# Kernel optimization log

Hardware: AMD Instinct MI355X
Metric: run time of the kernel (lower is better)

Reference implementation:

```python
import jax, jax.numpy as jnp
import numpy as np

B, CIN, COUT, WID, M1, M2, H, W = 8, 3, 3, 16, 8, 8, 256, 256


def _fftfreq(n, d):
    # torch.fft.fftfreq(n, d); d may be a traced scalar
    k = np.concatenate([np.arange(0, (n - 1) // 2 + 1), np.arange(-(n // 2), 0)]).astype(np.float32)
    return jnp.asarray(k) / (n * d)


def _cplx(ri):
    return jax.lax.complex(ri[..., 0], ri[..., 1])


def _inorm(v, eps=1e-5):
    # InstanceNorm2d, affine=False: normalize over spatial dims per (b, c)
    mu = jnp.mean(v, axis=(-2, -1), keepdims=True)
    var = jnp.var(v, axis=(-2, -1), keepdims=True)
    return (v - mu) * jax.lax.rsqrt(var + eps)


def setup_inputs() -> dict:
    key = jax.random.key(0)
    ks = jax.random.split(key, 13)
    scale = 1.0 / (WID * WID)
    u = lambda k, s: scale * (0.5 + 0.5 * jax.random.uniform(k, s, jnp.float32))
    return {
        "x": jax.random.normal(ks[0], (B, CIN, H, W), jnp.float32),
        "fc0_w": jax.random.normal(ks[1], (CIN + 2, WID), jnp.float32) * 0.1,
        "fc0_b": jax.random.normal(ks[2], (WID,), jnp.float32) * 0.01,
        "pole1_ri": u(ks[3], (WID, WID, M1, 2)),
        "pole2_ri": u(ks[4], (WID, WID, M2, 2)),
        "residue_ri": u(ks[5], (WID, WID, M1, M2, 2)),
        "w0_w": jax.random.normal(ks[6], (WID, WID), jnp.float32) * 0.1,
        "w0_b": jax.random.normal(ks[7], (WID,), jnp.float32) * 0.01,
        "fc1_w": jax.random.normal(ks[8], (WID, 128), jnp.float32) * 0.1,
        "fc1_b": jax.random.normal(ks[9], (128,), jnp.float32) * 0.01,
        "fc2_w": jax.random.normal(ks[10], (128, COUT), jnp.float32) * 0.1,
        "fc2_b": jax.random.normal(ks[11], (COUT,), jnp.float32) * 0.01,
        "tx": jnp.linspace(0.0, 1.0, W, dtype=jnp.float32).reshape(1, W),
        "ty": jnp.linspace(0.0, 1.0, H, dtype=jnp.float32).reshape(1, H),
    }


def _pr2d(v, p1, p2, res, tx, ty):
    # v: [b, i, h, w] real; p1:[i,k,m1], p2:[i,k,m2], res:[i,k,m1,m2] complex
    b, i, h, w = v.shape
    dty = ty[0, 1] - ty[0, 0]
    dtx = tx[0, 1] - tx[0, 0]
    alpha = jnp.fft.fft2(v)  # [b,i,h,w] complex64
    lam1 = (2j * jnp.pi) * _fftfreq(h, dty)  # [h]
    lam2 = (2j * jnp.pi) * _fftfreq(w, dtx)  # [w]
    A1 = 1.0 / (lam1[None, None, None, :] - p1[..., None])  # [i,k,p,h]
    A2 = 1.0 / (lam2[None, None, None, :] - p2[..., None])  # [i,k,q,w]
    # output_residue1[b,k,o,x] = sum_{i,p,q} alpha[b,i,o,x] res[i,k,p,q] A1[i,k,p,o] A2[i,k,q,x]
    T = jnp.einsum('ikpq,ikpo->ikqo', res, A1)
    G = jnp.einsum('ikqo,ikqx->ikox', T, A2)        # [i,k,h,w] pole-residue transfer kernel
    out1 = jnp.einsum('biox,ikox->bkox', alpha, G)
    x1 = jnp.fft.ifft2(out1).real
    # output_residue2[b,k,p,q] = sum_{i,o,x} alpha[b,i,o,x] res[i,k,p,q] A1[i,k,p,o] A2[i,k,q,x]
    S = jnp.einsum('biox,ikqx->bikoq', alpha, A2)
    Mt = jnp.einsum('bikoq,ikpo->bikpq', S, A1)
    out2 = jnp.einsum('bikpq,ikpq->bkpq', Mt, res)  # [b,k,m1,m2]
    # transient part: x2[n,i,z,x] = sum_{b,p,q} out2[n,b,p,q] exp(p1[b,i,p] ty[z]) exp(p2[b,i,q] tx[x])
    tyc = ty.reshape(-1).astype(p1.dtype)
    txc = tx.reshape(-1).astype(p2.dtype)
    E1 = jnp.exp(p1[..., None] * tyc)  # [i,k,p,h]
    E2 = jnp.exp(p2[..., None] * txc)  # [i,k,q,w]
    U = jnp.einsum('nbpq,bipz->nbiqz', out2, E1)
    x2 = jnp.einsum('nbiqz,biqx->nizx', U, E2).real / (w * h)
    return x1 + x2


def reference(x, fc0_w, fc0_b, pole1_ri, pole2_ri, residue_ri, w0_w, w0_b,
              fc1_w, fc1_b, fc2_w, fc2_b, tx, ty):
    b, c, h, w = x.shape
    v = jnp.transpose(x, (0, 2, 3, 1))  # [b,h,w,c]
    gx = jnp.broadcast_to(jnp.linspace(0.0, 1.0, h, dtype=x.dtype)[None, :, None, None], (b, h, w, 1))
    gy = jnp.broadcast_to(jnp.linspace(0.0, 1.0, w, dtype=x.dtype)[None, None, :, None], (b, h, w, 1))
    v = jnp.concatenate([v, gx, gy], axis=-1)
    v = v @ fc0_w + fc0_b                 # [b,h,w,width]
    v = jnp.transpose(v, (0, 3, 1, 2))    # [b,width,h,w]
    p1, p2, res = _cplx(pole1_ri), _cplx(pole2_ri), _cplx(residue_ri)
    x1 = _inorm(_pr2d(_inorm(v), p1, p2, res, tx, ty))
    x2 = jnp.einsum('bihw,oi->bohw', v, w0_w) + w0_b[None, :, None, None]  # 1x1 conv
    u = x1 + x2
    u = jnp.transpose(u, (0, 2, 3, 1))
    u = jnp.sin(u @ fc1_w + fc1_b)
    u = u @ fc2_w + fc2_b
    return jnp.transpose(u, (0, 3, 1, 2))
```

## Files before the change

### kernel.cpp

```cpp
#include <hip/hip_runtime.h>
#include <cstddef>

#define NPIX 65536
#define PI_F 3.14159265358979323846f

typedef float v4f __attribute__((ext_vector_type(4)));
typedef short v8s __attribute__((ext_vector_type(8)));
typedef unsigned short u16;

__device__ __forceinline__ void cacc(float2& acc, float2 a, float2 b) {
  acc.x = fmaf(a.x, b.x, fmaf(-a.y, b.y, acc.x));
  acc.y = fmaf(a.x, b.y, fmaf(a.y, b.x, acc.y));
}
__device__ __forceinline__ float2 cmulf(float2 a, float2 b) {
  return make_float2(a.x*b.x - a.y*b.y, a.x*b.y + a.y*b.x);
}
__device__ __forceinline__ float2 add2(float2 a, float2 b) { return make_float2(a.x+b.x, a.y+b.y); }
__device__ __forceinline__ float2 sub2(float2 a, float2 b) { return make_float2(a.x-b.x, a.y-b.y); }
__device__ __forceinline__ float2 shflc(float2 v, int mask) {
  return make_float2(__shfl_xor(v.x, mask), __shfl_xor(v.y, mask));
}
__device__ __forceinline__ void nts2(float2* p, float2 v) {
  __builtin_nontemporal_store(*reinterpret_cast<const double*>(&v),
                              reinterpret_cast<double*>(p));
}
__device__ __forceinline__ void nts1(float* p, float v) {
  __builtin_nontemporal_store(v, p);
}
__device__ __forceinline__ void bf16split(float v, u16& h, u16& l) {
  unsigned bits = __float_as_uint(v);
  h = (u16)(bits >> 16);
  float r = v - __uint_as_float((unsigned)h << 16);
  l = (u16)(__float_as_uint(r) >> 16);
}
__device__ __forceinline__ void make_tw(float sgn, int l, float2* tw) {
  const float c = sgn * (2.0f*PI_F/256.0f);
  int idxs[8] = { l, 64+l, 2*l, (l&31)<<2, (l&15)<<3, (l&7)<<4, (l&3)<<5, (l&1)<<6 };
  #pragma unroll
  for (int r = 0; r < 8; ++r) { float sn, cs; __sincosf(c*idxs[r], &sn, &cs); tw[r] = make_float2(cs, sn); }
}
__device__ __forceinline__ void fwd_stage(float2& vv, int lane, int H, float2 tws, bool unit) {
  float2 p = shflc(vv, H);
  bool up = (lane & H) != 0;
  float2 lo = add2(vv, p);
  float2 df = sub2(p, vv);
  float2 hi = unit ? df : cmulf(df, tws);
  vv = up ? hi : lo;
}
__device__ __forceinline__ void inv_stage(float2& vv, int lane, int H, float2 tws, bool unit) {
  float2 p = shflc(vv, H);
  bool up = (lane & H) != 0;
  float2 bv = up ? vv : p;
  float2 av = up ? p : vv;
  float2 t = unit ? bv : cmulf(bv, tws);
  vv = up ? sub2(av, t) : add2(av, t);
}
__device__ __forceinline__ void ifft256_reg(float2& v0, float2& v1, float2& v2,
    float2& v3, int lane, const float2* tw) {
  inv_stage(v0, lane, 1, tw[0], true ); inv_stage(v1, lane, 1, tw[0], true );
  inv_stage(v2, lane, 1, tw[0], true ); inv_stage(v3, lane, 1, tw[0], true );
  inv_stage(v0, lane, 2, tw[7], false); inv_stage(v1, lane, 2, tw[7], false);
  inv_stage(v2, lane, 2, tw[7], false); inv_stage(v3, lane, 2, tw[7], false);
  inv_stage(v0, lane, 4, tw[6], false); inv_stage(v1, lane, 4, tw[6], false);
  inv_stage(v2, lane, 4, tw[6], false); inv_stage(v3, lane, 4, tw[6], false);
  inv_stage(v0, lane, 8, tw[5], false); inv_stage(v1, lane, 8, tw[5], false);
  inv_stage(v2, lane, 8, tw[5], false); inv_stage(v3, lane, 8, tw[5], false);
  inv_stage(v0, lane, 16, tw[4], false); inv_stage(v1, lane, 16, tw[4], false);
  inv_stage(v2, lane, 16, tw[4], false); inv_stage(v3, lane, 16, tw[4], false);
  inv_stage(v0, lane, 32, tw[3], false); inv_stage(v1, lane, 32, tw[3], false);
  inv_stage(v2, lane, 32, tw[3], false); inv_stage(v3, lane, 32, tw[3], false);
  { float2 t01 = cmulf(v1, tw[2]); float2 n0 = add2(v0, t01), n1 = sub2(v0, t01);
    float2 t23 = cmulf(v3, tw[2]); float2 n2 = add2(v2, t23), n3 = sub2(v2, t23);
    v0 = n0; v1 = n1; v2 = n2; v3 = n3; }
  { float2 t02 = cmulf(v2, tw[0]); float2 n0 = add2(v0, t02), n2 = sub2(v0, t02);
    float2 t13 = cmulf(v3, tw[1]); float2 n1 = add2(v1, t13), n3 = sub2(v1, t13);
    v0 = n0; v2 = n2; v1 = n1; v3 = n3; }
}

__global__ __launch_bounds__(256) void k_setup(const float2* __restrict__ p1,
    const float2* __restrict__ p2, const float* __restrict__ txv,
    const float* __restrict__ tyv, float2* __restrict__ A1,
    float2* __restrict__ A2T, float2* __restrict__ A2L,
    float2* __restrict__ E1, float2* __restrict__ E2) {
  int gid = blockIdx.x*256 + threadIdx.x;
  int o = gid & 255, p = (gid>>8)&7, k = (gid>>11)&15, i = gid>>15;
  float ko = (o < 128) ? (float)o : (float)(o - 256);
  float dty = tyv[1] - tyv[0];
  float dtx = txv[1] - txv[0];
  const float TWO_PI = 6.283185307179586f;
  {
    float lam = TWO_PI * ko / (256.0f * dty);
    float2 pv = p1[(i*16+k)*8 + p];
    float xr = -pv.x, yi = lam - pv.y;
    float D = xr*xr + yi*yi;
    A1[((size_t)((i*16+k)*8 + p))*256 + o] = make_float2(xr/D, -yi/D);
    float tv = tyv[o];
    float m = expf(pv.x*tv);
    E1[((size_t)((i*16+k)*8 + p))*256 + o] = make_float2(m*cosf(pv.y*tv), m*sinf(pv.y*tv));
  }
  {
    int fo = __brev((unsigned)o) >> 24;
    float ko2 = (fo < 128) ? (float)fo : (float)(fo - 256);
    float lam = TWO_PI * ko2 / (256.0f * dtx);
    float2 pv = p2[(i*16+k)*8 + p];
    float xr = -pv.x, yi = lam - pv.y;
    float D = xr*xr + yi*yi;
    float2 val = make_float2(xr/D, -yi/D);
    A2T[((size_t)i*256 + o)*128 + k*8 + p] = val;
    A2L[((size_t)((i*16+k)*8 + p))*256 + o] = val;
    float tv = txv[o];
    float m = expf(pv.x*tv);
    E2[((size_t)((i*16+k)*8 + p))*256 + o] = make_float2(m*cosf(pv.y*tv), m*sinf(pv.y*tv));
  }
}

__global__ __launch_bounds__(256) void k_B(const float2* __restrict__ A2T,
    u16* __restrict__ BH, u16* __restrict__ BL) {
  int bid = blockIdx.x;
  int i = bid >> 3, g = bid & 7;
  int tid = threadIdx.x;
  int n2 = g*32 + (tid >> 3);
  int kq = n2 >> 1, par = n2 & 1;
  int x0 = (tid & 7) * 32;
  size_t outb = ((size_t)i*256 + n2)*512;
  for (int xx = 0; xx < 32; ++xx) {
    int x = x0 + xx;
    float2 a2 = A2T[((size_t)i*256 + x)*128 + kq];
    float v0 = par ? a2.y : a2.x;
    float v1 = par ? a2.x : -a2.y;
    u16 h0, l0, h1, l1;
    bf16split(v0, h0, l0);
    bf16split(v1, h1, l1);
    BH[outb + 2*x]     = h0;  BL[outb + 2*x]     = l0;
    BH[outb + 2*x + 1] = h1;  BL[outb + 2*x + 1] = l1;
  }
}

__global__ __launch_bounds__(256) void k_T(const float2* __restrict__ res,
    const float2* __restrict__ A1, float2* __restrict__ Tt) {
  int ik = blockIdx.x, tid = threadIdx.x;
  __shared__ float2 rbuf[64];
  __shared__ float2 a1[8][256];
  if (tid < 64) rbuf[tid] = res[(size_t)ik*64 + tid];
  for (int e = 0; e < 8; ++e) {
    int lin = tid + 256*e;
    int p = lin >> 8, o = lin & 255;
    a1[p][o] = A1[((size_t)ik*8 + p)*256 + o];
  }
  __syncthreads();
  int o = tid;
  #pragma unroll
  for (int q = 0; q < 8; ++q) {
    float2 acc = make_float2(0.f, 0.f);
    #pragma unroll
    for (int p = 0; p < 8; ++p) cacc(acc, rbuf[p*8+q], a1[p][o]);
    Tt[((size_t)ik*8 + q)*256 + o] = acc;
  }
}

__global__ __launch_bounds__(256) void k_stats_v_part(const float* __restrict__ x,
    const float* __restrict__ fc0w, const float* __restrict__ fc0b,
    float2* __restrict__ part) {
  int bid = blockIdx.x;
  int seg = bid & 7, img = bid >> 3;
  int k = img & 15, b = img >> 4;
  int tid = threadIdx.x;
  float w0 = fc0w[k], w1 = fc0w[16+k], w2 = fc0w[32+k], w3 = fc0w[48+k], w4 = fc0w[64+k];
  float base = fc0b[k] + (tid*(1.0f/255.0f))*w4;
  const float* xb = x + (size_t)b*3*NPIX + (size_t)seg*8192;
  float s = 0.f, s2 = 0.f;
  for (int it = 0; it < 32; ++it) {
    int row = seg*32 + it;
    int p = it*256 + tid;
    float val = base + (row*(1.0f/255.0f))*w3 + xb[p]*w0 + xb[NPIX+p]*w1 + xb[2*NPIX+p]*w2;
    s += val; s2 += val*val;
  }
  __shared__ float rs[256], rq[256];
  rs[tid] = s; rq[tid] = s2;
  __syncthreads();
  for (int off = 128; off > 0; off >>= 1) {
    if (tid < off) { rs[tid] += rs[tid+off]; rq[tid] += rq[tid+off]; }
    __syncthreads();
  }
  if (tid == 0) part[bid] = make_float2(rs[0], rq[0]);
}

__global__ __launch_bounds__(256) void k_stats_p_part(const float* __restrict__ v,
    float2* __restrict__ part) {
  int bid = blockIdx.x;
  int seg = bid & 7, img = bid >> 3;
  int tid = threadIdx.x;
  const float* p = v + (size_t)img*NPIX + (size_t)seg*8192;
  float s = 0.f, s2 = 0.f;
  for (int it = 0; it < 32; ++it) { float a = p[it*256 + tid]; s += a; s2 += a*a; }
  __shared__ float rs[256], rq[256];
  rs[tid] = s; rq[tid] = s2;
  __syncthreads();
  for (int off = 128; off > 0; off >>= 1) {
    if (tid < off) { rs[tid] += rs[tid+off]; rq[tid] += rq[tid+off]; }
    __syncthreads();
  }
  if (tid == 0) part[bid] = make_float2(rs[0], rq[0]);
}

__global__ __launch_bounds__(256) void k_stats_fin(const float2* __restrict__ part,
    float2* __restrict__ stats, int nimg) {
  int img = blockIdx.x*256 + threadIdx.x;
  if (img >= nimg) return;
  float s = 0.f, s2 = 0.f;
  #pragma unroll
  for (int e = 0; e < 8; ++e) { float2 v = part[img*8 + e]; s += v.x; s2 += v.y; }
  float mean = s * (1.0f/65536.0f);
  float var  = s2 * (1.0f/65536.0f) - mean*mean;
  stats[img] = make_float2(mean, rsqrtf(var + 1e-5f));
}

__global__ __launch_bounds__(256) void k_fft_v(const float* __restrict__ x,
    const float* __restrict__ fc0w, const float* __restrict__ fc0b,
    const float2* __restrict__ stats, float2* __restrict__ out) {
  int tid = threadIdx.x, lane = tid & 63, rowi = tid >> 6;
  int bid = blockIdx.x;
  int img = bid >> 6;
  int h   = (bid & 63)*4 + rowi;
  int k = img & 15, b = img >> 4;
  float2 st = stats[img];
  float w0 = fc0w[k], w1 = fc0w[16+k], w2 = fc0w[32+k], w3 = fc0w[48+k], w4 = fc0w[64+k];
  float bb = fc0b[k] + (h*(1.0f/255.0f))*w3;
  const float* xb = x + (size_t)b*3*NPIX + (size_t)h*256;
  float2 tw[8];
  make_tw(-1.0f, lane, tw);
  float2 v0, v1, v2, v3;
  {
    #pragma unroll
    for (int e = 0; e < 4; ++e) {
      int j = e*64 + lane;
      float val = bb + (j*(1.0f/255.0f))*w4 + xb[j]*w0 + xb[NPIX+j]*w1 + xb[2*NPIX+j]*w2;
      val = (val - st.x)*st.y;
      float2 c = make_float2(val, 0.f);
      if (e == 0) v0 = c; else if (e == 1) v1 = c; else if (e == 2) v2 = c; else v3 = c;
    }
  }
  { float2 n0 = add2(v0, v2), n2 = cmulf(sub2(v0, v2), tw[0]);
    float2 n1 = add2(v1, v3), n3 = cmulf(sub2(v1, v3), tw[1]);
    v0 = n0; v1 = n1; v2 = n2; v3 = n3; }
  { float2 n0 = add2(v0, v1), n1 = cmulf(sub2(v0, v1), tw[2]);
    float2 n2 = add2(v2, v3), n3 = cmulf(sub2(v2, v3), tw[2]);
    v0 = n0; v1 = n1; v2 = n2; v3 = n3; }
  fwd_stage(v0, lane, 32, tw[3], false); fwd_stage(v1, lane, 32, tw[3], false);
  fwd_stage(v2, lane, 32, tw[3], false); fwd_stage(v3, lane, 32, tw[3], false);
  fwd_stage(v0, lane, 16, tw[4], false); fwd_stage(v1, lane, 16, tw[4], false);
  fwd_stage(v2, lane, 16, tw[4], false); fwd_stage(v3, lane, 16, tw[4], false);
  fwd_stage(v0, lane,  8, tw[5], false); fwd_stage(v1, lane,  8, tw[5], false);
  fwd_stage(v2, lane,  8, tw[5], false); fwd_stage(v3, lane,  8, tw[5], false);
  fwd_stage(v0, lane,  4, tw[6], false); fwd_stage(v1, lane,  4, tw[6], false);
  fwd_stage(v2, lane,  4, tw[6], false); fwd_stage(v3, lane,  4, tw[6], false);
  fwd_stage(v0, lane,  2, tw[7], false); fwd_stage(v1, lane,  2, tw[7], false);
  fwd_stage(v2, lane,  2, tw[7], false); fwd_stage(v3, lane,  2, tw[7], false);
  fwd_stage(v0, lane,  1, tw[0], true ); fwd_stage(v1, lane,  1, tw[0], true );
  fwd_stage(v2, lane,  1, tw[0], true ); fwd_stage(v3, lane,  1, tw[0], true );
  float2* op = out + ((size_t)img*256 + h)*256;
  nts2(&op[lane], v0); nts2(&op[64+lane], v1);
  nts2(&op[128+lane], v2); nts2(&op[192+lane], v3);
}

__global__ __launch_bounds__(256) void k_fft_colR(const float2* __restrict__ in,
    float2* __restrict__ outp) {
  __shared__ float tr[256][17], tim[256][17];
  __shared__ float twr[128], twi[128];
  int tid = threadIdx.x;
  int c = tid & 15, g = tid >> 4;
  int img = blockIdx.x >> 4;
  int c0  = (blockIdx.x & 15) * 16;
  if (tid < 128) {
    float ang = (PI_F/128.0f)*tid;
    twr[tid] = cosf(ang); twi[tid] = -sinf(ang);
  }
  const float2* base = in + (size_t)img*NPIX + c0;
  #pragma unroll
  for (int it = 0; it < 16; ++it) {
    int row = it*16 + g;
    float2 v = base[(size_t)row*256 + c];
    int br = __brev((unsigned)row) >> 24;
    tr[br][c] = v.x; tim[br][c] = v.y;
  }
  __syncthreads();
  int lane = tid & 63, w = tid >> 6;
  int cw = w*4 + (lane >> 4);
  int gw = lane & 15;
  for (int s = 0; s < 8; ++s) {
    __builtin_amdgcn_wave_barrier();
    int half = 1 << s;
    #pragma unroll
    for (int r = 0; r < 8; ++r) {
      int m  = gw + 16*r;
      int t  = m & (half - 1);
      int grp = m >> s;
      int i0 = (grp << (s+1)) + t;
      int i1 = i0 + half;
      int twx = t << (7 - s);
      float wr = twr[twx], wi = twi[twx];
      float br = tr[i1][cw], bi = tim[i1][cw];
      float vr = br*wr - bi*wi, vi = br*wi + bi*wr;
      float ar = tr[i0][cw], ai = tim[i0][cw];
      tr[i0][cw] = ar + vr; tim[i0][cw] = ai + vi;
      tr[i1][cw] = ar - vr; tim[i1][cw] = ai - vi;
    }
  }
  __syncthreads();
  #pragma unroll
  for (int it = 0; it < 16; ++it) {
    int row = it*16 + g;
    float2 vv = make_float2(tr[row][c], tim[row][c]);
    nts2(&outp[((size_t)row*128 + img)*256 + c0 + c], vv);
  }
}

__global__ __launch_bounds__(256) void k_ifft_col_real(const float2* __restrict__ in,
    float* __restrict__ outp, float scale) {
  __shared__ float tr[256][17], tim[256][17];
  __shared__ float twr[128], twi[128];
  int tid = threadIdx.x;
  int c = tid & 15, g = tid >> 4;
  int img = blockIdx.x >> 4;
  int c0  = (blockIdx.x & 15) * 16;
  if (tid < 128) {
    float ang = (PI_F/128.0f)*tid;
    twr[tid] = cosf(ang); twi[tid] = sinf(ang);
  }
  const float2* base = in + (size_t)img*NPIX + c0;
  #pragma unroll
  for (int it = 0; it < 16; ++it) {
    int row = it*16 + g;
    float2 v = base[(size_t)row*256 + c];
    int br = __brev((unsigned)row) >> 24;
    tr[br][c] = v.x; tim[br][c] = v.y;
  }
  __syncthreads();
  int lane = tid & 63, w = tid >> 6;
  int cw = w*4 + (lane >> 4);
  int gw = lane & 15;
  for (int s = 0; s < 8; ++s) {
    __builtin_amdgcn_wave_barrier();
    int half = 1 << s;
    #pragma unroll
    for (int r = 0; r < 8; ++r) {
      int m  = gw + 16*r;
      int t  = m & (half - 1);
      int grp = m >> s;
      int i0 = (grp << (s+1)) + t;
      int i1 = i0 + half;
      int twx = t << (7 - s);
      float wr = twr[twx], wi = twi[twx];
      float br = tr[i1][cw], bi = tim[i1][cw];
      float vr = br*wr - bi*wi, vi = br*wi + bi*wr;
      float ar = tr[i0][cw], ai = tim[i0][cw];
      tr[i0][cw] = ar + vr; tim[i0][cw] = ai + vi;
      tr[i1][cw] = ar - vr; tim[i1][cw] = ai - vi;
    }
  }
  __syncthreads();
  float* ob = outp + (size_t)img*NPIX + c0;
  #pragma unroll
  for (int it = 0; it < 16; ++it) {
    int row = it*16 + g;
    nts1(&ob[(size_t)row*256 + c], tr[row][c]*scale);
  }
}

__global__ __launch_bounds__(256) void k_Smm(const float2* __restrict__ alphaR,
    const u16* __restrict__ BH, const u16* __restrict__ BL,
    float* __restrict__ Sf) {
  __shared__ u16 Ah[128][40], Al[128][40], Bhs[128][40], Bls[128][40];
  int bid = blockIdx.x;
  int i = bid >> 5, rem = bid & 31, mt = rem >> 1, nt = rem & 1;
  int tid = threadIdx.x;
  int lane = tid & 63, wid = tid >> 6, wr = wid >> 1, wc = wid & 1;
  int r2 = tid >> 1, h2 = tid & 1;
  int m_s = mt*128 + r2;
  const float2* arow = alphaR + ((size_t)((m_s & 255)*128) + (size_t)((m_s >> 8)*16 + i))*256 + h2*8;
  const u16* bhrow = BH + ((size_t)i*256 + nt*128 + r2)*512 + h2*16;
  const u16* blrow = BL + ((size_t)i*256 + nt*128 + r2)*512 + h2*16;
  v4f acc[4][4];
  #pragma unroll
  for (int a = 0; a < 4; ++a)
    #pragma unroll
    for (int b = 0; b < 4; ++b) acc[a][b] = (v4f){0.f, 0.f, 0.f, 0.f};
  for (int kc = 0; kc < 16; ++kc) {
    const float2* ap = arow + kc*16;
    #pragma unroll
    for (int e = 0; e < 8; ++e) {
      float2 v = ap[e];
      u16 hr, lr, hi_, li_;
      bf16split(v.x, hr, lr);
      bf16split(v.y, hi_, li_);
      int c = h2*16 + 2*e;
      Ah[r2][c] = hr; Ah[r2][c+1] = hi_;
      Al[r2][c] = lr; Al[r2][c+1] = li_;
    }
    {
      const uint4* ph = (const uint4*)(bhrow + (size_t)kc*32);
      uint4 q0 = ph[0], q1 = ph[1];
      *((uint4*)&Bhs[r2][h2*16])     = q0;
      *((uint4*)&Bhs[r2][h2*16 + 8]) = q1;
      const uint4* pl = (const uint4*)(blrow + (size_t)kc*32);
      uint4 s0 = pl[0], s1 = pl[1];
      *((uint4*)&Bls[r2][h2*16])     = s0;
      *((uint4*)&Bls[r2][h2*16 + 8]) = s1;
    }
    __syncthreads();
    v8s af_h[4], af_l[4];
    int c8 = (lane >> 4) * 8;
    #pragma unroll
    for (int fi = 0; fi < 4; ++fi) {
      int row = wr*64 + fi*16 + (lane & 15);
      af_h[fi] = *(const v8s*)&Ah[row][c8];
      af_l[fi] = *(const v8s*)&Al[row][c8];
    }
    #pragma unroll
    for (int fj = 0; fj < 4; ++fj) {
      int row = wc*64 + fj*16 + (lane & 15);
      v8s bh_f = *(const v8s*)&Bhs[row][c8];
      v8s bl_f = *(const v8s*)&Bls[row][c8];
      #pragma unroll
      for (int fi = 0; fi < 4; ++fi) {
        acc[fi][fj] = __builtin_amdgcn_mfma_f32_16x16x32_bf16(af_h[fi], bh_f, acc[fi][fj], 0, 0, 0);
        acc[fi][fj] = __builtin_amdgcn_mfma_f32_16x16x32_bf16(af_l[fi], bh_f, acc[fi][fj], 0, 0, 0);
        acc[fi][fj] = __builtin_amdgcn_mfma_f32_16x16x32_bf16(af_h[fi], bl_f, acc[fi][fj], 0, 0, 0);
      }
    }
    __syncthreads();
  }
  #pragma unroll
  for (int fi = 0; fi < 4; ++fi) {
    #pragma unroll
    for (int rr = 0; rr < 4; ++rr) {
      int m = mt*128 + wr*64 + fi*16 + (lane >> 4)*4 + rr;
      int n = m >> 8, o = m & 255;
      float* srow = Sf + ((size_t)(n*16 + i)*256 + o)*256 + nt*128 + wc*64 + (lane & 15);
      #pragma unroll
      for (int fj = 0; fj < 4; ++fj)
        nts1(&srow[fj*16], acc[fi][fj][rr]);
    }
  }
}

__global__ __launch_bounds__(256) void k_Mt(const float2* __restrict__ S,
    const float2* __restrict__ A1, float2* __restrict__ Mt) {
  __shared__ float2 sl[8][258];
  __shared__ float2 a1l[8][258];
  __shared__ float2 part[4][64];
  int bid = blockIdx.x;
  int k = bid & 15, ni = bid >> 4;
  int i = ni & 15;
  int ik = i*16 + k;
  int tid = threadIdx.x;
  for (int e = 0; e < 8; ++e) {
    int lin = tid + 256*e;
    int o = lin >> 3, q = lin & 7;
    sl[q][o] = S[((size_t)ni*256 + o)*128 + k*8 + q];
  }
  for (int e = 0; e < 8; ++e) {
    int lin = tid + 256*e;
    int p = lin >> 8, o = lin & 255;
    a1l[p][o] = A1[((size_t)ik*8 + p)*256 + o];
  }
  __syncthreads();
  int oq = tid >> 6, pq = tid & 63, p = pq >> 3, q = pq & 7;
  float2 acc = make_float2(0.f, 0.f);
  int o0 = oq*64;
  for (int o = o0; o < o0 + 64; ++o) cacc(acc, sl[q][o], a1l[p][o]);
  part[oq][pq] = acc;
  __syncthreads();
  if (oq == 0) {
    float2 a = part[0][pq], b = part[1][pq], c = part[2][pq], d = part[3][pq];
    acc.x = a.x + b.x + c.x + d.x;
    acc.y = a.y + b.y + c.y + d.y;
    Mt[(size_t)bid*64 + pq] = acc;
  }
}

__global__ __launch_bounds__(256) void k_out2(const float2* __restrict__ Mt,
    const float2* __restrict__ res, float2* __restrict__ out2) {
  int gid = blockIdx.x*256 + threadIdx.x;
  int pq = gid & 63, k = (gid >> 6) & 15, n = gid >> 10;
  float2 acc = make_float2(0.f, 0.f);
  for (int i = 0; i < 16; ++i)
    cacc(acc, Mt[((size_t)((n*16+i)*16 + k))*64 + pq], res[((size_t)(i*16+k))*64 + pq]);
  out2[((size_t)(n*16+k))*64 + pq] = acc;
}

__global__ __launch_bounds__(256) void k_out1g(const float2* __restrict__ alphaR,
    const float2* __restrict__ Tt, const float2* __restrict__ A2L,
    float2* __restrict__ out1) {
  __shared__ float2 tl[2][128];
  __shared__ float sre[4][256], sim[4][256];
  int d = blockIdx.x;
  int xcd = d & 7, idx = d >> 3;
  int o  = xcd*32 + (idx >> 3);
  int kh = idx & 7;
  int tid = threadIdx.x, x = tid;
  int lane = tid & 63, rowi = tid >> 6;
  {
    int kk = tid >> 7, rem = tid & 127;
    int i = rem >> 3, q = rem & 7;
    tl[kk][rem] = Tt[((size_t)((i*16 + 2*kh + kk)*8 + q))*256 + o];
  }
  float2 tw[8];
  make_tw(+1.0f, lane, tw);
  __syncthreads();
  float2 g0[16], g1[16];
  #pragma unroll
  for (int i = 0; i < 16; ++i) {
    const float2* a2k0 = &A2L[((size_t)((i*16 + 2*kh + 0)*8))*256 + x];
    const float2* a2k1 = &A2L[((size_t)((i*16 + 2*kh + 1)*8))*256 + x];
    float2 acc0 = make_float2(0.f, 0.f), acc1 = make_float2(0.f, 0.f);
    #pragma unroll
    for (int q = 0; q < 8; ++q) {
      cacc(acc0, tl[0][i*8+q], a2k0[(size_t)q*256]);
      cacc(acc1, tl[1][i*8+q], a2k1[(size_t)q*256]);
    }
    g0[i] = acc0; g1[i] = acc1;
  }
  const float2* arow = alphaR + (size_t)o*128*256 + x;
  float2 arA[16], arB[16];
  #pragma unroll
  for (int i = 0; i < 16; ++i) arA[i] = arow[(size_t)(0*16 + i)*256];
  #pragma unroll
  for (int i = 0; i < 16; ++i) arB[i] = arow[(size_t)(1*16 + i)*256];
  for (int bp = 0; bp < 4; ++bp) {
    float2 acc0 = make_float2(0.f,0.f), acc1 = acc0, acc2 = acc0, acc3 = acc0;
    #pragma unroll
    for (int i = 0; i < 16; ++i) {
      cacc(acc0, arA[i], g0[i]);
      cacc(acc1, arA[i], g1[i]);
      cacc(acc2, arB[i], g0[i]);
      cacc(acc3, arB[i], g1[i]);
    }
    sre[0][x] = acc0.x; sim[0][x] = acc0.y;
    sre[1][x] = acc1.x; sim[1][x] = acc1.y;
    sre[2][x] = acc2.x; sim[2][x] = acc2.y;
    sre[3][x] = acc3.x; sim[3][x] = acc3.y;
    __syncthreads();
    if (bp < 3) {
      int b0 = (bp+1)*2, b1 = b0 + 1;
      #pragma unroll
      for (int i = 0; i < 16; ++i) arA[i] = arow[(size_t)(b0*16 + i)*256];
      #pragma unroll
      for (int i = 0; i < 16; ++i) arB[i] = arow[(size_t)(b1*16 + i)*256];
    }
    float2 v0 = make_float2(sre[rowi][lane],     sim[rowi][lane]);
    float2 v1 = make_float2(sre[rowi][64+lane],  sim[rowi][64+lane]);
    float2 v2 = make_float2(sre[rowi][128+lane], sim[rowi][128+lane]);
    float2 v3 = make_float2(sre[rowi][192+lane], sim[rowi][192+lane]);
    ifft256_reg(v0, v1, v2, v3, lane, tw);
    int img = (bp*2 + (rowi >> 1))*16 + 2*kh + (rowi & 1);
    float2* op = out1 + ((size_t)img*256 + o)*256;
    nts2(&op[lane], v0); nts2(&op[64+lane], v1);
    nts2(&op[128+lane], v2); nts2(&op[192+lane], v3);
    __syncthreads();
  }
}

__global__ __launch_bounds__(256) void k_x2t(const float2* __restrict__ out2,
    const float2* __restrict__ E1, const float2* __restrict__ E2,
    float* __restrict__ x1pre) {
  int bid = blockIdx.x;
  int zb = bid & 31, nk = bid >> 5;
  int kk = nk & 15, n = nk >> 4;
  int x = threadIdx.x;
  __shared__ float2 o2[1024];
  __shared__ float2 e1l[1024];
  __shared__ float2 ul[1024];
  for (int e = 0; e < 4; ++e) {
    int lin = threadIdx.x + 256*e;
    int j = lin >> 6, pq = lin & 63;
    o2[lin] = out2[((size_t)(n*16 + j))*64 + pq];
  }
  for (int e = 0; e < 4; ++e) {
    int lin = threadIdx.x + 256*e;
    int j = lin >> 6, p = (lin >> 3) & 7, zz = lin & 7;
    e1l[lin] = E1[(((size_t)(j*16 + kk))*8 + p)*256 + zb*8 + zz];
  }
  __syncthreads();
  for (int e = 0; e < 4; ++e) {
    int lin = threadIdx.x + 256*e;
    int j = lin >> 6, q = (lin >> 3) & 7, zz = lin & 7;
    float2 acc = make_float2(0.f, 0.f);
    #pragma unroll
    for (int p = 0; p < 8; ++p) cacc(acc, o2[j*64 + p*8 + q], e1l[j*64 + p*8 + zz]);
    ul[lin] = acc;
  }
  __syncthreads();
  float acc[8] = {0.f,0.f,0.f,0.f,0.f,0.f,0.f,0.f};
  const float2* e2b = E2 + (size_t)kk*2048 + x;
  float2 nxt = e2b[0];
  for (int jq = 0; jq < 128; ++jq) {
    float2 e2 = nxt;
    int njq = jq + 1;
    if (njq < 128) {
      int nj = njq >> 3, nq = njq & 7;
      nxt = e2b[(size_t)nj*32768 + (size_t)nq*256];
    }
    const float4* up4 = reinterpret_cast<const float4*>(&ul[jq*8]);
    float4 u01 = up4[0], u23 = up4[1], u45 = up4[2], u67 = up4[3];
    acc[0] = fmaf(u01.x, e2.x, fmaf(-u01.y, e2.y, acc[0]));
    acc[1] = fmaf(u01.z, e2.x, fmaf(-u01.w, e2.y, acc[1]));
    acc[2] = fmaf(u23.x, e2.x, fmaf(-u23.y, e2.y, acc[2]));
    acc[3] = fmaf(u23.z, e2.x, fmaf(-u23.w, e2.y, acc[3]));
    acc[4] = fmaf(u45.x, e2.x, fmaf(-u45.y, e2.y, acc[4]));
    acc[5] = fmaf(u45.z, e2.x, fmaf(-u45.w, e2.y, acc[5]));
    acc[6] = fmaf(u67.x, e2.x, fmaf(-u67.y, e2.y, acc[6]));
    acc[7] = fmaf(u67.z, e2.x, fmaf(-u67.w, e2.y, acc[7]));
  }
  const float sc = 1.0f/65536.0f;
  #pragma unroll
  for (int zz = 0; zz < 8; ++zz) {
    size_t idx = (((size_t)nk)*256 + zb*8 + zz)*256 + x;
    x1pre[idx] += acc[zz]*sc;
  }
}

__global__ __launch_bounds__(256) void k_final(const float* __restrict__ x,
    const float* __restrict__ x1pre, const float2* __restrict__ stats2,
    const float* __restrict__ fc0w, const float* __restrict__ fc0b,
    const float* __restrict__ w0w, const float* __restrict__ w0b,
    const float* __restrict__ fc1w, const float* __restrict__ fc1b,
    const float* __restrict__ fc2w, const float* __restrict__ fc2b,
    float* __restrict__ out) {
  __shared__ float s_fc1w[2048], s_fc1b[128], s_fc2w[384], s_w0w[256], s_w0b[16], s_fc2b[3];
  int tid = threadIdx.x;
  for (int e = 0; e < 8; ++e) s_fc1w[tid + 256*e] = fc1w[tid + 256*e];
  if (tid < 128) s_fc1b[tid] = fc1b[tid];
  for (int e = 0; e < 2; ++e) { int q = tid + 256*e; if (q < 384) s_fc2w[q] = fc2w[q]; }
  s_w0w[tid] = w0w[tid];
  if (tid < 16) s_w0b[tid] = w0b[tid];
  if (tid < 3)  s_fc2b[tid] = fc2b[tid];
  __syncthreads();

  int bid = blockIdx.x;
  int hh = bid & 255, b = bid >> 8;
  int ww = tid;
  size_t pix = (size_t)hh*256 + ww;
  float xc0 = x[((size_t)b*3 + 0)*NPIX + pix];
  float xc1 = x[((size_t)b*3 + 1)*NPIX + pix];
  float xc2 = x[((size_t)b*3 + 2)*NPIX + pix];
  float gx = hh*(1.0f/255.0f), gy = ww*(1.0f/255.0f);
  float v[16], x1n[16], uo[16];
  #pragma unroll
  for (int k = 0; k < 16; ++k)
    v[k] = fc0b[k] + xc0*fc0w[k] + xc1*fc0w[16+k] + xc2*fc0w[32+k] + gx*fc0w[48+k] + gy*fc0w[64+k];
  #pragma unroll
  for (int k = 0; k < 16; ++k) {
    float2 st = stats2[b*16 + k];
    float xv = x1pre[((size_t)(b*16 + k))*NPIX + pix];
    x1n[k] = (xv - st.x)*st.y;
  }
  #pragma unroll
  for (int o = 0; o < 16; ++o) {
    float acc = s_w0b[o];
    #pragma unroll
    for (int k = 0; k < 16; ++k) acc = fmaf(v[k], s_w0w[o*16+k], acc);
    uo[o] = acc + x1n[o];
  }
  float o0 = 0.f, o1 = 0.f, o2 = 0.f;
  for (int jj = 0; jj < 128; ++jj) {
    float t = s_fc1b[jj];
    #pragma unroll
    for (int k = 0; k < 16; ++k) t = fmaf(uo[k], s_fc1w[k*128 + jj], t);
    float s = __sinf(t);
    o0 = fmaf(s, s_fc2w[jj*3+0], o0);
    o1 = fmaf(s, s_fc2w[jj*3+1], o1);
    o2 = fmaf(s, s_fc2w[jj*3+2], o2);
  }
  out[((size_t)b*3 + 0)*NPIX + pix] = o0 + s_fc2b[0];
  out[((size_t)b*3 + 1)*NPIX + pix] = o1 + s_fc2b[1];
  out[((size_t)b*3 + 2)*NPIX + pix] = o2 + s_fc2b[2];
}

extern "C" void kernel_launch(void* const* d_in, const int* in_sizes, int n_in,
                              void* d_out, int out_size, void* d_ws, size_t ws_size,
                              hipStream_t stream) {
  const float*  x    = (const float*)d_in[0];
  const float*  fc0w = (const float*)d_in[1];
  const float*  fc0b = (const float*)d_in[2];
  const float2* p1   = (const float2*)d_in[3];
  const float2* p2   = (const float2*)d_in[4];
  const float2* res  = (const float2*)d_in[5];
  const float*  w0w  = (const float*)d_in[6];
  const float*  w0b  = (const float*)d_in[7];
  const float*  fc1w = (const float*)d_in[8];
  const float*  fc1b = (const float*)d_in[9];
  const float*  fc2w = (const float*)d_in[10];
  const float*  fc2b = (const float*)d_in[11];
  const float*  txv  = (const float*)d_in[12];
  const float*  tyv  = (const float*)d_in[13];
  float* out = (float*)d_out;

  const size_t OFF_A1   = 0;
  const size_t OFF_A2T  = 4194304;
  const size_t OFF_E1   = 8388608;
  const size_t OFF_E2   = 12582912;
  const size_t OFF_ST1  = 16777216;
  const size_t OFF_ST2  = 16778240;
  const size_t OFF_OUT2 = 16779264;
  const size_t OFF_MT   = 16844800;
  const size_t OFF_S    = 17893376;
  const size_t OFF_X1   = 51447808;
  const size_t OFF_A    = 85002240;
  const size_t OFF_B    = 152111104;
  const size_t OFF_G    = 219219968;
  const size_t NEED     = 252774400;
  if (ws_size < NEED) return;
  char* ws = (char*)d_ws;
  float2* A1  = (float2*)(ws + OFF_A1);
  float2* A2T = (float2*)(ws + OFF_A2T);
  float2* E1  = (float2*)(ws + OFF_E1);
  float2* E2  = (float2*)(ws + OFF_E2);
  float2* st1 = (float2*)(ws + OFF_ST1);
  float2* st2 = (float2*)(ws + OFF_ST2);
  float2* o2b = (float2*)(ws + OFF_OUT2);
  float2* Mt  = (float2*)(ws + OFF_MT);
  float2* Sb  = (float2*)(ws + OFF_S);
  float2* Tt  = (float2*)(ws + OFF_X1);
  float*  X1  = (float*)(ws + OFF_X1);
  float2* Ab  = (float2*)(ws + OFF_A);
  float2* Bb  = (float2*)(ws + OFF_B);
  float2* A2L = (float2*)(ws + OFF_G);
  u16*    BH  = (u16*)(ws + OFF_G + 4194304);
  u16*    BL  = (u16*)(ws + OFF_G + 8388608);

  k_setup  <<<2048, 256, 0, stream>>>(p1, p2, txv, tyv, A1, A2T, A2L, E1, E2);
  k_B      <<<128, 256, 0, stream>>>(A2T, BH, BL);
  k_T      <<<256, 256, 0, stream>>>(res, A1, Tt);
  k_stats_v_part<<<1024, 256, 0, stream>>>(x, fc0w, fc0b, Sb);
  k_stats_fin   <<<1, 256, 0, stream>>>(Sb, st1, 128);
  k_fft_v  <<<8192, 256, 0, stream>>>(x, fc0w, fc0b, st1, Ab);
  k_fft_colR<<<2048, 256, 0, stream>>>(Ab, Bb);
  k_Smm    <<<512, 256, 0, stream>>>(Bb, BH, BL, (float*)Sb);
  k_Mt     <<<2048, 256, 0, stream>>>(Sb, A1, Mt);
  k_out2   <<<32, 256, 0, stream>>>(Mt, res, o2b);
  k_out1g  <<<2048, 256, 0, stream>>>(Bb, Tt, A2L, Ab);
  k_ifft_col_real<<<2048, 256, 0, stream>>>(Ab, X1, 1.0f/65536.0f);
  k_x2t    <<<4096, 256, 0, stream>>>(o2b, E1, E2, X1);
  k_stats_p_part<<<1024, 256, 0, stream>>>(X1, Sb);
  k_stats_fin   <<<1, 256, 0, stream>>>(Sb, st2, 128);
  k_final  <<<2048, 256, 0, stream>>>(x, X1, st2, fc0w, fc0b,
                                      w0w, w0b, fc1w, fc1b, fc2w, fc2b, out);
}
```

Before: 519.9 us.

## Move x2 exponential-sum contraction to split-bf16 MFMA matmul

Replaces the scalar FMA k_x2t kernel with a two-stage path. k_Umm forms U and stores it split into bf16 high/low parts, and k_E2s pre-splits E2 the same way. k_x2tmm then runs a 256x256x128 complex-as-real GEMM per batch using three bf16 MFMAs to approximate fp32 precision. k_out1g also double-buffers its shared staging arrays so one of its barriers can be dropped. The cost is extra workspace traffic for the split operands, and the stats scratch buffer moves to Mt so it no longer clashes with the reused Sb region.

Measured after the change: 502.0 us. 3.4% less time.

```diff
diff --git a/kernel.cpp b/kernel.cpp
--- a/kernel.cpp
+++ b/kernel.cpp
@@ -133,6 +133,22 @@
     bf16split(v1, h1, l1);
     BH[outb + 2*x]     = h0;  BL[outb + 2*x]     = l0;
     BH[outb + 2*x + 1] = h1;  BL[outb + 2*x + 1] = l1;
+  }
+}
+
+__global__ __launch_bounds__(256) void k_E2s(const float2* __restrict__ E2,
+    unsigned* __restrict__ EH32, unsigned* __restrict__ EL32) {
+  int kk = blockIdx.x;
+  int x = threadIdx.x;
+  for (int jq = 0; jq < 128; ++jq) {
+    int j = jq >> 3, q = jq & 7;
+    float2 e2 = E2[(((size_t)(j*16 + kk))*8 + q)*256 + x];
+    u16 h0,l0,h1,l1;
+    bf16split(e2.x, h0, l0);
+    bf16split(-e2.y, h1, l1);
+    size_t idx = ((size_t)kk*256 + x)*128 + jq;
+    EH32[idx] = (unsigned)h0 | ((unsigned)h1 << 16);
+    EL32[idx] = (unsigned)l0 | ((unsigned)l1 << 16);
   }
 }
 
@@ -489,11 +505,133 @@
   out2[((size_t)(n*16+k))*64 + pq] = acc;
 }
 
+__global__ __launch_bounds__(256) void k_Umm(const float2* __restrict__ out2,
+    const float2* __restrict__ E1, unsigned* __restrict__ UH32,
+    unsigned* __restrict__ UL32) {
+  __shared__ float2 o2l[1024];
+  __shared__ float2 ul[64][129];
+  int batch = blockIdx.x;
+  int kk = batch & 15, n = batch >> 4;
+  int tid = threadIdx.x, lane = tid & 63, w = tid >> 6;
+  for (int e = 0; e < 4; ++e) {
+    int lin = tid + 256*e;
+    int j = lin >> 6, pq = lin & 63;
+    o2l[lin] = out2[((size_t)(n*16 + j))*64 + pq];
+  }
+  __syncthreads();
+  for (int zc = 0; zc < 4; ++zc) {
+    int z = zc*64 + lane;
+    #pragma unroll
+    for (int jj = 0; jj < 4; ++jj) {
+      int j = w*4 + jj;
+      float2 e1r[8];
+      #pragma unroll
+      for (int p = 0; p < 8; ++p)
+        e1r[p] = E1[(((size_t)(j*16 + kk))*8 + p)*256 + z];
+      #pragma unroll
+      for (int q = 0; q < 8; ++q) {
+        float2 acc = make_float2(0.f,0.f);
+        #pragma unroll
+        for (int p = 0; p < 8; ++p) cacc(acc, o2l[j*64 + p*8 + q], e1r[p]);
+        ul[lane][j*8+q] = acc;
+      }
+    }
+    __syncthreads();
+    int jq = tid & 127, zh = tid >> 7;
+    for (int it = 0; it < 32; ++it) {
+      int zz = zh*32 + it;
+      float2 u = ul[zz][jq];
+      u16 hr, lr, hi_, li_;
+      bf16split(u.x, hr, lr);
+      bf16split(u.y, hi_, li_);
+      size_t idx = ((size_t)batch*256 + zc*64 + zz)*128 + jq;
+      UH32[idx] = (unsigned)hr | ((unsigned)hi_ << 16);
+      UL32[idx] = (unsigned)lr | ((unsigned)li_ << 16);
+    }
+    __syncthreads();
+  }
+}
+
+__global__ __launch_bounds__(256) void k_x2tmm(const u16* __restrict__ UH,
+    const u16* __restrict__ UL, const u16* __restrict__ EH,
+    const u16* __restrict__ EL, float* __restrict__ X1) {
+  __shared__ u16 Ah[128][40], Al[128][40], Bhs[128][40], Bls[128][40];
+  int bid = blockIdx.x;
+  int batch = bid >> 2, mt = (bid >> 1) & 1, nt = bid & 1;
+  int kk = batch & 15;
+  int tid = threadIdx.x;
+  int lane = tid & 63, wid = tid >> 6, wr = wid >> 1, wc = wid & 1;
+  int r2 = tid >> 1, h2 = tid & 1;
+  const u16* uhrow = UH + ((size_t)(batch*256 + mt*128 + r2))*256 + h2*16;
+  const u16* ulrow = UL + ((size_t)(batch*256 + mt*128 + r2))*256 + h2*16;
+  const u16* ehrow = EH + ((size_t)(kk*256 + nt*128 + r2))*256 + h2*16;
+  const u16* elrow = EL + ((size_t)(kk*256 + nt*128 + r2))*256 + h2*16;
+  v4f acc[4][4];
+  #pragma unroll
+  for (int a = 0; a < 4; ++a)
+    #pragma unroll
+    for (int b = 0; b < 4; ++b) acc[a][b] = (v4f){0.f, 0.f, 0.f, 0.f};
+  for (int kc = 0; kc < 8; ++kc) {
+    {
+      const uint4* pa = (const uint4*)(uhrow + (size_t)kc*32);
+      uint4 a0 = pa[0], a1 = pa[1];
+      *((uint4*)&Ah[r2][h2*16])     = a0;
+      *((uint4*)&Ah[r2][h2*16 + 8]) = a1;
+      const uint4* pb = (const uint4*)(ulrow + (size_t)kc*32);
+      uint4 b0 = pb[0], b1 = pb[1];
+      *((uint4*)&Al[r2][h2*16])     = b0;
+      *((uint4*)&Al[r2][h2*16 + 8]) = b1;
+      const uint4* pc = (const uint4*)(ehrow + (size_t)kc*32);
+      uint4 c0 = pc[0], c1 = pc[1];
+      *((uint4*)&Bhs[r2][h2*16])     = c0;
+      *((uint4*)&Bhs[r2][h2*16 + 8]) = c1;
+      const uint4* pd = (const uint4*)(elrow + (size_t)kc*32);
+      uint4 d0 = pd[0], d1 = pd[1];
+      *((uint4*)&Bls[r2][h2*16])     = d0;
+      *((uint4*)&Bls[r2][h2*16 + 8]) = d1;
+    }
+    __syncthreads();
+    v8s af_h[4], af_l[4];
+    int c8 = (lane >> 4) * 8;
+    #pragma unroll
+    for (int fi = 0; fi < 4; ++fi) {
+      int row = wr*64 + fi*16 + (lane & 15);
+      af_h[fi] = *(const v8s*)&Ah[row][c8];
+      af_l[fi] = *(const v8s*)&Al[row][c8];
+    }
+    #pragma unroll
+    for (int fj = 0; fj < 4; ++fj) {
+      int row = wc*64 + fj*16 + (lane & 15);
+      v8s bh_f = *(const v8s*)&Bhs[row][c8];
+      v8s bl_f = *(const v8s*)&Bls[row][c8];
+      #pragma unroll
+      for (int fi = 0; fi < 4; ++fi) {
+        acc[fi][fj] = __builtin_amdgcn_mfma_f32_16x16x32_bf16(af_h[fi], bh_f, acc[fi][fj], 0, 0, 0);
+        acc[fi][fj] = __builtin_amdgcn_mfma_f32_16x16x32_bf16(af_l[fi], bh_f, acc[fi][fj], 0, 0, 0);
+        acc[fi][fj] = __builtin_amdgcn_mfma_f32_16x16x32_bf16(af_h[fi], bl_f, acc[fi][fj], 0, 0, 0);
+      }
+    }
+    __syncthreads();
+  }
+  const float sc = 1.0f/65536.0f;
+  #pragma unroll
+  for (int fi = 0; fi < 4; ++fi) {
+    #pragma unroll
+    for (int rr = 0; rr < 4; ++rr) {
+      int z = mt*128 + wr*64 + fi*16 + (lane >> 4)*4 + rr;
+      float* row = X1 + (size_t)batch*NPIX + (size_t)z*256 + nt*128 + wc*64 + (lane & 15);
+      #pragma unroll
+      for (int fj = 0; fj < 4; ++fj)
+        row[fj*16] += acc[fi][fj][rr] * sc;
+    }
+  }
+}
+
 __global__ __launch_bounds__(256) void k_out1g(const float2* __restrict__ alphaR,
     const float2* __restrict__ Tt, const float2* __restrict__ A2L,
     float2* __restrict__ out1) {
   __shared__ float2 tl[2][128];
-  __shared__ float sre[4][256], sim[4][256];
+  __shared__ float sre[2][4][256], sim[2][4][256];
   int d = blockIdx.x;
   int xcd = d & 7, idx = d >> 3;
   int o  = xcd*32 + (idx >> 3);
@@ -528,6 +666,7 @@
   #pragma unroll
   for (int i = 0; i < 16; ++i) arB[i] = arow[(size_t)(1*16 + i)*256];
   for (int bp = 0; bp < 4; ++bp) {
+    int pb = bp & 1;
     float2 acc0 = make_float2(0.f,0.f), acc1 = acc0, acc2 = acc0, acc3 = acc0;
     #pragma unroll
     for (int i = 0; i < 16; ++i) {
@@ -536,10 +675,10 @@
       cacc(acc2, arB[i], g0[i]);
       cacc(acc3, arB[i], g1[i]);
     }
-    sre[0][x] = acc0.x; sim[0][x] = acc0.y;
-    sre[1][x] = acc1.x; sim[1][x] = acc1.y;
-    sre[2][x] = acc2.x; sim[2][x] = acc2.y;
-    sre[3][x] = acc3.x; sim[3][x] = acc3.y;
+    sre[pb][0][x] = acc0.x; sim[pb][0][x] = acc0.y;
+    sre[pb][1][x] = acc1.x; sim[pb][1][x] = acc1.y;
+    sre[pb][2][x] = acc2.x; sim[pb][2][x] = acc2.y;
+    sre[pb][3][x] = acc3.x; sim[pb][3][x] = acc3.y;
     __syncthreads();
     if (bp < 3) {
       int b0 = (bp+1)*2, b1 = b0 + 1;
@@ -548,75 +687,15 @@
       #pragma unroll
       for (int i = 0; i < 16; ++i) arB[i] = arow[(size_t)(b1*16 + i)*256];
     }
-    float2 v0 = make_float2(sre[rowi][lane],     sim[rowi][lane]);
-    float2 v1 = make_float2(sre[rowi][64+lane],  sim[rowi][64+lane]);
-    float2 v2 = make_float2(sre[rowi][128+lane], sim[rowi][128+lane]);
-    float2 v3 = make_float2(sre[rowi][192+lane], sim[rowi][192+lane]);
+    float2 v0 = make_float2(sre[pb][rowi][lane],     sim[pb][rowi][lane]);
+    float2 v1 = make_float2(sre[pb][rowi][64+lane],  sim[pb][rowi][64+lane]);
+    float2 v2 = make_float2(sre[pb][rowi][128+lane], sim[pb][rowi][128+lane]);
+    float2 v3 = make_float2(sre[pb][rowi][192+lane], sim[pb][rowi][192+lane]);
     ifft256_reg(v0, v1, v2, v3, lane, tw);
     int img = (bp*2 + (rowi >> 1))*16 + 2*kh + (rowi & 1);
     float2* op = out1 + ((size_t)img*256 + o)*256;
     nts2(&op[lane], v0); nts2(&op[64+lane], v1);
     nts2(&op[128+lane], v2); nts2(&op[192+lane], v3);
-    __syncthreads();
-  }
-}
-
-__global__ __launch_bounds__(256) void k_x2t(const float2* __restrict__ out2,
-    const float2* __restrict__ E1, const float2* __restrict__ E2,
-    float* __restrict__ x1pre) {
-  int bid = blockIdx.x;
-  int zb = bid & 31, nk = bid >> 5;
-  int kk = nk & 15, n = nk >> 4;
-  int x = threadIdx.x;
-  __shared__ float2 o2[1024];
-  __shared__ float2 e1l[1024];
-  __shared__ float2 ul[1024];
-  for (int e = 0; e < 4; ++e) {
-    int lin = threadIdx.x + 256*e;
-    int j = lin >> 6, pq = lin & 63;
-    o2[lin] = out2[((size_t)(n*16 + j))*64 + pq];
-  }
-  for (int e = 0; e < 4; ++e) {
-    int lin = threadIdx.x + 256*e;
-    int j = lin >> 6, p = (lin >> 3) & 7, zz = lin & 7;
-    e1l[lin] = E1[(((size_t)(j*16 + kk))*8 + p)*256 + zb*8 + zz];
-  }
-  __syncthreads();
-  for (int e = 0; e < 4; ++e) {
-    int lin = threadIdx.x + 256*e;
-    int j = lin >> 6, q = (lin >> 3) & 7, zz = lin & 7;
-    float2 acc = make_float2(0.f, 0.f);
-    #pragma unroll
-    for (int p = 0; p < 8; ++p) cacc(acc, o2[j*64 + p*8 + q], e1l[j*64 + p*8 + zz]);
-    ul[lin] = acc;
-  }
-  __syncthreads();
-  float acc[8] = {0.f,0.f,0.f,0.f,0.f,0.f,0.f,0.f};
-  const float2* e2b = E2 + (size_t)kk*2048 + x;
-  float2 nxt = e2b[0];
-  for (int jq = 0; jq < 128; ++jq) {
-    float2 e2 = nxt;
-    int njq = jq + 1;
-    if (njq < 128) {
-      int nj = njq >> 3, nq = njq & 7;
-      nxt = e2b[(size_t)nj*32768 + (size_t)nq*256];
-    }
-    const float4* up4 = reinterpret_cast<const float4*>(&ul[jq*8]);
-    float4 u01 = up4[0], u23 = up4[1], u45 = up4[2], u67 = up4[3];
-    acc[0] = fmaf(u01.x, e2.x, fmaf(-u01.y, e2.y, acc[0]));
-    acc[1] = fmaf(u01.z, e2.x, fmaf(-u01.w, e2.y, acc[1]));
-    acc[2] = fmaf(u23.x, e2.x, fmaf(-u23.y, e2.y, acc[2]));
-    acc[3] = fmaf(u23.z, e2.x, fmaf(-u23.w, e2.y, acc[3]));
-    acc[4] = fmaf(u45.x, e2.x, fmaf(-u45.y, e2.y, acc[4]));
-    acc[5] = fmaf(u45.z, e2.x, fmaf(-u45.w, e2.y, acc[5]));
-    acc[6] = fmaf(u67.x, e2.x, fmaf(-u67.y, e2.y, acc[6]));
-    acc[7] = fmaf(u67.z, e2.x, fmaf(-u67.w, e2.y, acc[7]));
-  }
-  const float sc = 1.0f/65536.0f;
-  #pragma unroll
-  for (int zz = 0; zz < 8; ++zz) {
-    size_t idx = (((size_t)nk)*256 + zb*8 + zz)*256 + x;
-    x1pre[idx] += acc[zz]*sc;
   }
 }
 
@@ -728,9 +807,14 @@
   float2* A2L = (float2*)(ws + OFF_G);
   u16*    BH  = (u16*)(ws + OFF_G + 4194304);
   u16*    BL  = (u16*)(ws + OFF_G + 8388608);
+  unsigned* EH32 = (unsigned*)(ws + OFF_G + 12582912);
+  unsigned* EL32 = (unsigned*)(ws + OFF_G + 14680064);
+  unsigned* UH32 = (unsigned*)(ws + OFF_S);
+  unsigned* UL32 = (unsigned*)(ws + OFF_S + 16777216);
 
   k_setup  <<<2048, 256, 0, stream>>>(p1, p2, txv, tyv, A1, A2T, A2L, E1, E2);
   k_B      <<<128, 256, 0, stream>>>(A2T, BH, BL);
+  k_E2s    <<<16, 256, 0, stream>>>(E2, EH32, EL32);
   k_T      <<<256, 256, 0, stream>>>(res, A1, Tt);
   k_stats_v_part<<<1024, 256, 0, stream>>>(x, fc0w, fc0b, Sb);
   k_stats_fin   <<<1, 256, 0, stream>>>(Sb, st1, 128);
@@ -739,11 +823,13 @@
   k_Smm    <<<512, 256, 0, stream>>>(Bb, BH, BL, (float*)Sb);
   k_Mt     <<<2048, 256, 0, stream>>>(Sb, A1, Mt);
   k_out2   <<<32, 256, 0, stream>>>(Mt, res, o2b);
+  k_Umm    <<<128, 256, 0, stream>>>(o2b, E1, UH32, UL32);
   k_out1g  <<<2048, 256, 0, stream>>>(Bb, Tt, A2L, Ab);
   k_ifft_col_real<<<2048, 256, 0, stream>>>(Ab, X1, 1.0f/65536.0f);
-  k_x2t    <<<4096, 256, 0, stream>>>(o2b, E1, E2, X1);
-  k_stats_p_part<<<1024, 256, 0, stream>>>(X1, Sb);
-  k_stats_fin   <<<1, 256, 0, stream>>>(Sb, st2, 128);
+  k_x2tmm  <<<512, 256, 0, stream>>>((const u16*)UH32, (const u16*)UL32,
+                                     (const u16*)EH32, (const u16*)EL32, X1);
+  k_stats_p_part<<<1024, 256, 0, stream>>>(X1, Mt);
+  k_stats_fin   <<<1, 256, 0, stream>>>(Mt, st2, 128);
   k_final  <<<2048, 256, 0, stream>>>(x, X1, st2, fc0w, fc0b,
                                       w0w, w0b, fc1w, fc1b, fc2w, fc2b, out);
 }
```
